# Kernel optimization log

Hardware: AMD Instinct MI355X
Metric: run time of the kernel (lower is better)

Reference implementation:

```python
import jax, jax.numpy as jnp
import numpy as np

K = 5            # SplineConv kernel_size per dim, dim=3
KC = K ** 3      # 125 weight matrices
N0, N1, N2, N3 = 32768, 8192, 2048, 512   # node counts per pooling level (8 graphs)
E0, E1, E2, E3 = 262144, 65536, 16384, 4096
B = 8
NV = B * 8       # dense 2x2x2 voxel grid per graph -> fc1 input 8*256


def spline_conv(x, edge_index, pseudo, W, root, bias):
    # degree-1 (linear) open B-spline convolution, mean aggregation,
    # plus root weight and bias (torch SplineConv defaults).
    src, dst = edge_index[0], edge_index[1]
    N, Cin = x.shape
    Kc, _, Cout = W.shape
    E = src.shape[0]
    v = pseudo * (K - 1)                               # [E,3]
    lo = jnp.clip(jnp.floor(v), 0, K - 2)
    frac = v - lo                                      # [E,3]
    lo = lo.astype(jnp.int32)
    bits = jnp.array([[(s >> d) & 1 for d in range(3)] for s in range(8)], dtype=jnp.int32)  # [8,3]
    idx = lo[:, None, :] + bits[None]                  # [E,8,3] corner grid indices
    w = jnp.where(bits[None] == 1, frac[:, None, :], 1.0 - frac[:, None, :])
    bw = jnp.prod(w, axis=-1)                          # [E,8] basis weights (sum to 1)
    kidx = idx[..., 0] + K * idx[..., 1] + K * K * idx[..., 2]  # [E,8] flat kernel index
    if N * Kc < E * Cin:
        # project every node through all 125 kernels, then gather per edge-corner
        P = jnp.einsum('nc,kco->nko', x, W)            # [N,125,Cout]
        msg = jnp.sum(bw[..., None] * P[src[:, None], kidx], axis=1)  # [E,Cout]
    else:
        # gather weight matrices per edge-corner (cheaper when Cin small)
        xs = x[src]                                    # [E,Cin]
        msg = jnp.zeros((E, Cout), x.dtype)
        for s in range(8):                             # fixed 8 corners of trilinear basis
            msg = msg + bw[:, s, None] * jnp.einsum('ec,eco->eo', xs, W[kidx[:, s]])
    agg = jax.ops.segment_sum(msg, dst, num_segments=N)
    deg = jax.ops.segment_sum(jnp.ones((E,), x.dtype), dst, num_segments=N)
    return agg / jnp.maximum(deg, 1.0)[:, None] + x @ root + bias


def pool_max(x, cluster, n_out):
    out = jax.ops.segment_max(x, cluster, num_segments=n_out)
    return jnp.where(jnp.isfinite(out), out, 0.0)      # empty voxels -> 0


def setup_inputs():
    key = jax.random.key(0)
    ks = iter(jax.random.split(key, 40))
    inp = {"x": jax.random.normal(next(ks), (N0, 1), jnp.float32)}
    levels = [(E0, N0, N1), (E1, N1, N2), (E2, N2, N3), (E3, N3, NV)]
    for l, (E, N, Nn) in enumerate(levels, start=1):
        inp[f"edge_index{l}"] = jax.random.randint(next(ks), (2, E), 0, N)
        inp[f"pseudo{l}"] = jax.random.uniform(next(ks), (E, 3), dtype=jnp.float32)
        inp[f"cluster{l}"] = jax.random.randint(next(ks), (N,), 0, Nn)
    chans = [(1, 32), (32, 64), (64, 128), (128, 256)]
    for l, (ci, co) in enumerate(chans, start=1):
        inp[f"W{l}"] = jax.random.normal(next(ks), (KC, ci, co), jnp.float32) / np.sqrt(ci * 8.0)
        inp[f"root{l}"] = jax.random.normal(next(ks), (ci, co), jnp.float32) / np.sqrt(float(ci))
        inp[f"b{l}"] = jnp.zeros((co,), jnp.float32)
    inp["fc1_w"] = jax.random.normal(next(ks), (2048, 512), jnp.float32) / np.sqrt(2048.0)
    inp["fc1_b"] = jnp.zeros((512,), jnp.float32)
    inp["fc2_w"] = jax.random.normal(next(ks), (512, 10), jnp.float32) / np.sqrt(512.0)
    inp["fc2_b"] = jnp.zeros((10,), jnp.float32)
    return inp


def reference(x, edge_index1, pseudo1, cluster1, edge_index2, pseudo2, cluster2,
              edge_index3, pseudo3, cluster3, edge_index4, pseudo4, cluster4,
              W1, root1, b1, W2, root2, b2, W3, root3, b3, W4, root4, b4,
              fc1_w, fc1_b, fc2_w, fc2_b):
    h = jax.nn.elu(spline_conv(x, edge_index1, pseudo1, W1, root1, b1))
    h = pool_max(h, cluster1, N1)                      # sparse voxel max pool 0.02
    h = jax.nn.elu(spline_conv(h, edge_index2, pseudo2, W2, root2, b2))
    h = pool_max(h, cluster2, N2)                      # sparse voxel max pool 0.04
    h = jax.nn.elu(spline_conv(h, edge_index3, pseudo3, W3, root3, b3))
    h = pool_max(h, cluster3, N3)                      # sparse voxel max pool 0.08
    h = jax.nn.elu(spline_conv(h, edge_index4, pseudo4, W4, root4, b4))
    h = pool_max(h, cluster4, NV)                      # dense 2x2x2 voxel max pool
    h = h.reshape(B, 8 * 256)
    h = jax.nn.elu(h @ fc1_w + fc1_b)                  # dropout is identity in eval mode
    return jax.nn.log_softmax(h @ fc2_w + fc2_b, axis=1)
```

## Files before the change

### kernel.cpp

```cpp
#include <hip/hip_runtime.h>

typedef __attribute__((ext_vector_type(8))) short bf16x8;
typedef __attribute__((ext_vector_type(4))) float f32x4;
typedef __attribute__((ext_vector_type(4))) unsigned short us4;
typedef __attribute__((ext_vector_type(8))) unsigned short us8;

#define DEVI __device__ __forceinline__

#define MAXW2 1088
#define MAXW3 640
#define MAXW4 512


DEVI unsigned enc_pool(float f) {
  unsigned u = __float_as_uint(f);
  return (u & 0x80000000u) ? ~u : (u | 0x80000000u);
}
DEVI float dec_pool(unsigned k) {
  if (k == 0u) return 0.0f;
  return __uint_as_float((k & 0x80000000u) ? (k ^ 0x80000000u) : ~k);
}
DEVI float eluf(float x) { return x > 0.0f ? x : expm1f(x); }
DEVI unsigned short to_bf16(float f) {
  unsigned u = __float_as_uint(f);
  return (unsigned short)((u + 0x7FFFu + ((u >> 16) & 1u)) >> 16);
}

struct Basis { float bw[8]; int kidx[8]; int cell; };

DEVI Basis make_basis(const float* __restrict__ ps, int e) {
  Basis bs;
  float f[3]; int lo[3];
#pragma unroll
  for (int d = 0; d < 3; ++d) {
    float v = ps[e * 3 + d] * 4.0f;
    float fl = fminf(fmaxf(floorf(v), 0.0f), 3.0f);
    lo[d] = (int)fl;
    f[d] = v - fl;
  }
  bs.cell = lo[0] + 4 * lo[1] + 16 * lo[2];
#pragma unroll
  for (int s = 0; s < 8; ++s) {
    int b0 = s & 1, b1 = (s >> 1) & 1, b2 = (s >> 2) & 1;
    bs.bw[s] = (b0 ? f[0] : 1.0f - f[0]) * (b1 ? f[1] : 1.0f - f[1]) *
               (b2 ? f[2] : 1.0f - f[2]);
    bs.kidx[s] = (lo[0] + b0) + 5 * (lo[1] + b1) + 25 * (lo[2] + b2);
  }
  return bs;
}

DEVI int cell_of(const float* __restrict__ ps, int e) {
  int cell = 0;
#pragma unroll
  for (int d = 0; d < 3; ++d) {
    float v = ps[e * 3 + d] * 4.0f;
    float fl = fminf(fmaxf(floorf(v), 0.0f), 3.0f);
    cell |= ((int)fl) << (2 * d);
  }
  return cell;
}

template <int CIN, int COUT>
DEVI void convw(const float* __restrict__ W, unsigned short* __restrict__ P, int idx) {
  constexpr int MAT = CIN * COUT;
  int k = idx / MAT, off = idx % MAT;
  int j = off & 7, g = (off >> 3) & 3;
  int rem = off >> 5;
  int n = rem % COUT, kb = rem / COUT;
  int c = kb * 32 + g * 8 + j;
  P[idx] = to_bf16(W[(k * CIN + c) * COUT + n]);
}

__global__ __launch_bounds__(256) void sc_prep(
    const float* __restrict__ W2, const float* __restrict__ W3, const float* __restrict__ W4,
    unsigned short* __restrict__ P2, unsigned short* __restrict__ P3, unsigned short* __restrict__ P4,
    const int* __restrict__ ei2, const float* __restrict__ ps2,
    const int* __restrict__ ei3, const float* __restrict__ ps3,
    const int* __restrict__ ei4, const float* __restrict__ ps4,
    unsigned* __restrict__ bc2, unsigned* __restrict__ bc3, unsigned* __restrict__ bc4,
    unsigned* __restrict__ deg2, unsigned* __restrict__ deg3, unsigned* __restrict__ deg4,
    const float* __restrict__ x, const int* __restrict__ ei1, const float* __restrict__ ps1,
    const float* __restrict__ W1, float* __restrict__ agg1, unsigned* __restrict__ deg1) {
  __shared__ unsigned hist[64];
  int b = blockIdx.x, t = threadIdx.x;
  if (b < 1000) { convw<32, 64>(W2, P2, b * 256 + t); return; }
  b -= 1000;
  if (b < 4000) { convw<64, 128>(W3, P3, b * 256 + t); return; }
  b -= 4000;
  if (b < 16000) { convw<128, 256>(W4, P4, b * 256 + t); return; }
  b -= 16000;
  if (b < 336) {
    const int* ei; const float* ps; unsigned *bc, *deg; int E, blk, NB;
    if (b < 256)      { ei = ei2; ps = ps2; bc = bc2; deg = deg2; E = 65536; blk = b;       NB = 256; }
    else if (b < 320) { ei = ei3; ps = ps3; bc = bc3; deg = deg3; E = 16384; blk = b - 256; NB = 64;  }
    else              { ei = ei4; ps = ps4; bc = bc4; deg = deg4; E = 4096;  blk = b - 320; NB = 16;  }
    if (t < 64) hist[t] = 0;
    __syncthreads();
    int e = blk * 256 + t;
    atomicAdd(&hist[cell_of(ps, e)], 1u);
    atomicAdd(deg + ei[E + e], 1u);
    __syncthreads();
    if (t < 64) bc[(size_t)t * NB + blk] = hist[t];
    return;
  }
  b -= 336;
  int tid = b * 256 + t;
  int e = tid >> 5, o = tid & 31;
  int src = ei1[e], dst = ei1[262144 + e];
  Basis bs = make_basis(ps1, e);
  float acc = 0.f;
#pragma unroll
  for (int s = 0; s < 8; ++s) acc += bs.bw[s] * W1[bs.kidx[s] * 32 + o];
  atomicAdd(agg1 + dst * 32 + o, x[src] * acc);
  if (o == 0) atomicAdd(deg1 + dst, 1u);
}

__global__ __launch_bounds__(1024) void sc_scan_all(
    const unsigned* __restrict__ bc2, const unsigned* __restrict__ bc3,
    const unsigned* __restrict__ bc4,
    unsigned* __restrict__ bb2, unsigned* __restrict__ bb3, unsigned* __restrict__ bb4,
    unsigned* __restrict__ cnt2, unsigned* __restrict__ cnt3, unsigned* __restrict__ cnt4,
    unsigned* __restrict__ base2, unsigned* __restrict__ base3, unsigned* __restrict__ base4,
    unsigned* __restrict__ wt2, unsigned* __restrict__ wt3, unsigned* __restrict__ wt4) {
  __shared__ unsigned tot[3][64];
  __shared__ unsigned sbs[3][64];
  int t = threadIdx.x, w = t >> 6, lane = t & 63;
#pragma unroll
  for (int lvl = 0; lvl < 3; ++lvl) {
    const unsigned* bc = lvl == 0 ? bc2 : lvl == 1 ? bc3 : bc4;
    unsigned* bb = lvl == 0 ? bb2 : lvl == 1 ? bb3 : bb4;
    int NB = lvl == 0 ? 256 : lvl == 1 ? 64 : 16;
    for (int c = w; c < 64; c += 16) {
      unsigned cellsum = 0;
      for (int sub = 0; sub * 64 < NB; ++sub) {
        int bi = sub * 64 + lane;
        unsigned v = (bi < NB) ? bc[c * NB + bi] : 0u;
        int incl = (int)v;
#pragma unroll
        for (int d = 1; d < 64; d <<= 1) {
          int tv = __shfl_up(incl, d);
          if (lane >= d) incl += tv;
        }
        if (bi < NB) bb[c * NB + bi] = cellsum + (unsigned)incl - v;
        cellsum += (unsigned)__shfl(incl, 63);
      }
      if (lane == 0) tot[lvl][c] = cellsum;
    }
  }
  __syncthreads();
  if (w < 3) {
    unsigned* cnt = w == 0 ? cnt2 : w == 1 ? cnt3 : cnt4;
    unsigned* bs  = w == 0 ? base2 : w == 1 ? base3 : base4;
    unsigned* wt  = w == 0 ? wt2 : w == 1 ? wt3 : wt4;
    int NSP  = w == 0 ? 1 : w == 1 ? 2 : 4;
    int MAXW = w == 0 ? MAXW2 : w == 1 ? MAXW3 : MAXW4;
    unsigned v = tot[w][lane];
    int incl = (int)v;
#pragma unroll
    for (int d = 1; d < 64; d <<= 1) {
      int tv = __shfl_up(incl, d);
      if (lane >= d) incl += tv;
    }
    unsigned excl = (unsigned)incl - v;
    sbs[w][lane] = excl;
    cnt[lane] = v;
    bs[lane] = excl;
    int nch = (int)((v + 63) >> 6);
    int cscan = nch;
#pragma unroll
    for (int d = 1; d < 64; d <<= 1) {
      int tv = __shfl_up(cscan, d);
      if (lane >= d) cscan += tv;
    }
    int cbase = cscan - nch;
    int CT = __shfl(cscan, 63);
    for (int ch = 0; ch < nch; ++ch)
      for (int ns = 0; ns < NSP; ++ns)
        wt[(cbase + ch) * NSP + ns] = ((unsigned)lane << 16) | ((unsigned)ch << 8) | (unsigned)ns;
    for (int i = CT * NSP + lane; i < MAXW; i += 64) wt[i] = 0xFFFFFFFFu;
  }
  __syncthreads();
  for (int i = t; i < 64 * 256; i += 1024) bb2[i] += sbs[0][i >> 8];
  for (int i = t; i < 64 * 64; i += 1024)  bb3[i] += sbs[1][i >> 6];
  for (int i = t; i < 64 * 16; i += 1024)  bb4[i] += sbs[2][i >> 4];
}

__global__ __launch_bounds__(256) void sc_rank_fin1(
    const int* __restrict__ ei2, const float* __restrict__ ps2,
    const int* __restrict__ ei3, const float* __restrict__ ps3,
    const int* __restrict__ ei4, const float* __restrict__ ps4,
    const unsigned* __restrict__ bb2, const unsigned* __restrict__ bb3,
    const unsigned* __restrict__ bb4,
    int* __restrict__ pos2, int* __restrict__ pos3, int* __restrict__ pos4,
    int* __restrict__ dst2, int* __restrict__ dst3, int* __restrict__ dst4,
    const float* __restrict__ x, const float* __restrict__ agg1,
    const unsigned* __restrict__ deg1, const float* __restrict__ root1,
    const float* __restrict__ b1, const int* __restrict__ cl1,
    unsigned* __restrict__ pe1) {
  __shared__ unsigned hist[64];
  int b = blockIdx.x, t = threadIdx.x;
  if (b < 336) {
    const int* ei; const float* ps; const unsigned* bb; int *pos, *dsts; int E, blk, NB;
    if (b < 256)      { ei = ei2; ps = ps2; bb = bb2; pos = pos2; dsts = dst2; E = 65536; blk = b;       NB = 256; }
    else if (b < 320) { ei = ei3; ps = ps3; bb = bb3; pos = pos3; dsts = dst3; E = 16384; blk = b - 256; NB = 64;  }
    else              { ei = ei4; ps = ps4; bb = bb4; pos = pos4; dsts = dst4; E = 4096;  blk = b - 320; NB = 16;  }
    if (t < 64) hist[t] = 0;
    __syncthreads();
    int e = blk * 256 + t;
    int cell = cell_of(ps, e);
    unsigned r = atomicAdd(&hist[cell], 1u);
    int p = (int)(bb[cell * NB + blk] + r);
    pos[e] = p;
    dsts[p] = ei[E + e];
    return;
  }
  b -= 336;
  int tid = b * 256 + t;
  int n = tid >> 5, o = tid & 31;
  unsigned dv = deg1[n];
  float acc = agg1[tid] / (float)(dv ? dv : 1u) + b1[o] + x[n] * root1[o];
  atomicMax(pe1 + (size_t)cl1[n] * 32 + o, enc_pool(eluf(acc)));
}

template <int CIN, int COUT>
__global__ void sc_finpool(const unsigned* __restrict__ xenc, const float* __restrict__ agg,
                           const unsigned* __restrict__ deg, const float* __restrict__ root,
                           const float* __restrict__ bias, const int* __restrict__ cluster,
                           unsigned* __restrict__ pe_out, int N) {
  int tid = blockIdx.x * blockDim.x + threadIdx.x;
  if (tid >= N * COUT) return;
  int n = tid / COUT, o = tid % COUT;
  unsigned dv = deg[n];
  float acc = agg[tid] / (float)(dv ? dv : 1u) + bias[o];
#pragma unroll 4
  for (int c = 0; c < CIN; ++c)
    acc += dec_pool(xenc[n * CIN + c]) * root[c * COUT + o];
  atomicMax(pe_out + (size_t)cluster[n] * COUT + o, enc_pool(eluf(acc)));
}

template <int CIN>
__global__ void sc_fill(const unsigned* __restrict__ xenc, const int* __restrict__ ei,
                        const float* __restrict__ ps, const int* __restrict__ posb,
                        unsigned short* __restrict__ A, int E) {
  int gid = blockIdx.x * blockDim.x + threadIdx.x;
  int e = gid >> 6, lane = gid & 63;
  if (e >= E) return;
  int src = ei[e];
  int p = posb[e];
  float f[3];
#pragma unroll
  for (int d = 0; d < 3; ++d) {
    float v = ps[e * 3 + d] * 4.0f;
    float fl = fminf(fmaxf(floorf(v), 0.0f), 3.0f);
    f[d] = v - fl;
  }
  int sB = lane >> 3;
  int b0 = sB & 1, b1 = (sB >> 1) & 1, b2 = sB >> 2;
  float b = (b0 ? f[0] : 1.0f - f[0]) * (b1 ? f[1] : 1.0f - f[1]) *
            (b2 ? f[2] : 1.0f - f[2]);
  constexpr int K = 8 * CIN;
  if (CIN == 32) {
    uint4 xv = *(const uint4*)(xenc + (size_t)src * 32 + (lane & 7) * 4);
    us4 o;
    o[0] = to_bf16(b * dec_pool(xv.x)); o[1] = to_bf16(b * dec_pool(xv.y));
    o[2] = to_bf16(b * dec_pool(xv.z)); o[3] = to_bf16(b * dec_pool(xv.w));
    *(us4*)(A + (size_t)p * K + lane * 4) = o;
  } else if (CIN == 64) {
    const uint4* xp = (const uint4*)(xenc + (size_t)src * 64 + (lane & 7) * 8);
    uint4 xa = xp[0], xb = xp[1];
    us8 o;
    o[0] = to_bf16(b * dec_pool(xa.x)); o[1] = to_bf16(b * dec_pool(xa.y));
    o[2] = to_bf16(b * dec_pool(xa.z)); o[3] = to_bf16(b * dec_pool(xa.w));
    o[4] = to_bf16(b * dec_pool(xb.x)); o[5] = to_bf16(b * dec_pool(xb.y));
    o[6] = to_bf16(b * dec_pool(xb.z)); o[7] = to_bf16(b * dec_pool(xb.w));
    *(us8*)(A + (size_t)p * K + lane * 8) = o;
  } else {
    const uint4* xp = (const uint4*)(xenc + (size_t)src * 128 + (lane & 7) * 16);
#pragma unroll
    for (int h = 0; h < 2; ++h) {
      uint4 xa = xp[h * 2], xb = xp[h * 2 + 1];
      us8 o;
      o[0] = to_bf16(b * dec_pool(xa.x)); o[1] = to_bf16(b * dec_pool(xa.y));
      o[2] = to_bf16(b * dec_pool(xa.z)); o[3] = to_bf16(b * dec_pool(xa.w));
      o[4] = to_bf16(b * dec_pool(xb.x)); o[5] = to_bf16(b * dec_pool(xb.y));
      o[6] = to_bf16(b * dec_pool(xb.z)); o[7] = to_bf16(b * dec_pool(xb.w));
      *(us8*)(A + (size_t)p * K + lane * 16 + h * 8) = o;
    }
  }
}

template <int CIN, int COUT, int NSP>
DEVI void gemm_impl(const unsigned short* __restrict__ A, const unsigned short* __restrict__ Wp,
                    const unsigned* __restrict__ cnt, const unsigned* __restrict__ base,
                    const unsigned* __restrict__ wtab, const int* __restrict__ dsts,
                    float* __restrict__ agg) {
  constexpr int K = 8 * CIN;
  constexpr int NCOL = COUT / NSP;
  constexpr int NT = NCOL / 16;
  constexpr int UPT = NCOL / 32;
  constexpr int NPASS = K / 64;
  __shared__ __attribute__((aligned(16))) unsigned char lds[2 * NCOL * 80];
  unsigned u = wtab[blockIdx.x];
  if (u == 0xFFFFFFFFu) return;
  int cell = u >> 16, chunk = (u >> 8) & 255, nsl = u & 255;
  int n0 = nsl * NCOL;
  int m = (int)cnt[cell], cb = (int)base[cell];
  int row0 = chunk * 64;
  int tid = threadIdx.x;
  int wv = tid >> 6, lane = tid & 63, g4 = lane >> 4, ln = lane & 15;
  int lo0 = cell & 3, lo1 = (cell >> 2) & 3, lo2 = cell >> 4;
  int arow = cb + min(row0 + wv * 16 + ln, m - 1);
  f32x4 acc[NT];
#pragma unroll
  for (int t = 0; t < NT; ++t) acc[t] = (f32x4){0.f, 0.f, 0.f, 0.f};
  for (int pass = 0; pass < NPASS; ++pass) {
    int k0 = pass * 64;
    __syncthreads();
#pragma unroll
    for (int i = 0; i < UPT; ++i) {
      int u16 = tid + i * 256;
      int grp = u16 / (4 * NCOL), win = u16 % (4 * NCOL);
      int kg = k0 + grp * 32;
      int s = kg / CIN, kb = (kg % CIN) >> 5;
      int b0 = s & 1, b1 = (s >> 1) & 1, b2 = (s >> 2) & 1;
      int mat = (lo0 + b0) + 5 * (lo1 + b1) + 25 * (lo2 + b2);
      const us8* srcp = (const us8*)(Wp + (size_t)mat * (CIN * COUT) +
                                     (size_t)(kb * COUT * 4 + n0 * 4 + win) * 8);
      int r = grp * NCOL + (win >> 2), gg = win & 3;
      *(us8*)(lds + r * 80 + gg * 16) = *srcp;
    }
    __syncthreads();
#pragma unroll
    for (int kk = 0; kk < 2; ++kk) {
      bf16x8 af = *(const bf16x8*)(A + (size_t)arow * K + k0 + kk * 32 + g4 * 8);
#pragma unroll
      for (int t = 0; t < NT; ++t) {
        int r = kk * NCOL + t * 16 + ln;
        bf16x8 bfr = *(const bf16x8*)(lds + r * 80 + g4 * 16);
        acc[t] = __builtin_amdgcn_mfma_f32_16x16x32_bf16(af, bfr, acc[t], 0, 0, 0);
      }
    }
  }
  int row_b = row0 + wv * 16 + g4 * 4;
  int dstv[4];
#pragma unroll
  for (int r4 = 0; r4 < 4; ++r4)
    dstv[r4] = (row_b + r4 < m) ? dsts[cb + row_b + r4] : -1;
#pragma unroll
  for (int t = 0; t < NT; ++t) {
#pragma unroll
    for (int r4 = 0; r4 < 4; ++r4) {
      if (dstv[r4] >= 0)
        atomicAdd(agg + (size_t)dstv[r4] * COUT + n0 + t * 16 + ln, acc[t][r4]);
    }
  }
}

__global__ __launch_bounds__(256) void sc_gemm_l2(
    const unsigned short* A, const unsigned short* Wp, const unsigned* cnt,
    const unsigned* base, const unsigned* wtab, const int* dsts, float* agg) {
  gemm_impl<32, 64, 1>(A, Wp, cnt, base, wtab, dsts, agg);
}
__global__ __launch_bounds__(256) void sc_gemm_l3(
    const unsigned short* A, const unsigned short* Wp, const unsigned* cnt,
    const unsigned* base, const unsigned* wtab, const int* dsts, float* agg) {
  gemm_impl<64, 128, 2>(A, Wp, cnt, base, wtab, dsts, agg);
}
__global__ __launch_bounds__(256) void sc_gemm_l4(
    const unsigned short* A, const unsigned short* Wp, const unsigned* cnt,
    const unsigned* base, const unsigned* wtab, const int* dsts, float* agg) {
  gemm_impl<128, 256, 4>(A, Wp, cnt, base, wtab, dsts, agg);
}

__global__ void sc_fc1(const unsigned* __restrict__ xenc, const float* __restrict__ w,
                       float* __restrict__ out) {
  __shared__ float sx[8][32];
  int t = threadIdx.x;
  int j = blockIdx.x * 256 + t;
  int c0 = blockIdx.y * 32;
  {
    int b = t >> 5, c = t & 31;
    sx[b][c] = dec_pool(xenc[b * 2048 + c0 + c]);
  }
  __syncthreads();
  float acc[8];
#pragma unroll
  for (int b = 0; b < 8; ++b) acc[b] = 0.f;
#pragma unroll 4
  for (int cc = 0; cc < 32; ++cc) {
    float wv = w[(size_t)(c0 + cc) * 512 + j];
#pragma unroll
    for (int b = 0; b < 8; ++b) acc[b] += sx[b][cc] * wv;
  }
#pragma unroll
  for (int b = 0; b < 8; ++b) atomicAdd(out + b * 512 + j, acc[b]);
}

__global__ void sc_fc2(const float* __restrict__ h, const float* __restrict__ b1,
                       const float* __restrict__ w2, const float* __restrict__ b2,
                       float* __restrict__ out) {
  int b = blockIdx.x;
  int lane = threadIdx.x;
  float part[10];
#pragma unroll
  for (int o = 0; o < 10; ++o) part[o] = 0.f;
  for (int k = 0; k < 8; ++k) {
    int c = k * 64 + lane;
    float v = eluf(h[b * 512 + c] + b1[c]);
#pragma unroll
    for (int o = 0; o < 10; ++o) part[o] += v * w2[c * 10 + o];
  }
#pragma unroll
  for (int o = 0; o < 10; ++o) {
#pragma unroll
    for (int d = 32; d > 0; d >>= 1) part[o] += __shfl_down(part[o], d);
  }
  if (lane == 0) {
    float z[10], mx = -1e30f;
#pragma unroll
    for (int o = 0; o < 10; ++o) { z[o] = part[o] + b2[o]; mx = fmaxf(mx, z[o]); }
    float sum = 0.f;
#pragma unroll
    for (int o = 0; o < 10; ++o) sum += expf(z[o] - mx);
    float lse = mx + logf(sum);
#pragma unroll
    for (int o = 0; o < 10; ++o) out[b * 10 + o] = z[o] - lse;
  }
}

extern "C" void kernel_launch(void* const* d_in, const int* in_sizes, int n_in,
                              void* d_out, int out_size, void* d_ws, size_t ws_size,
                              hipStream_t stream) {
  (void)in_sizes; (void)n_in; (void)out_size; (void)ws_size;
  const float* x    = (const float*)d_in[0];
  const int*   ei1  = (const int*)d_in[1];
  const float* ps1  = (const float*)d_in[2];
  const int*   cl1  = (const int*)d_in[3];
  const int*   ei2  = (const int*)d_in[4];
  const float* ps2  = (const float*)d_in[5];
  const int*   cl2  = (const int*)d_in[6];
  const int*   ei3  = (const int*)d_in[7];
  const float* ps3  = (const float*)d_in[8];
  const int*   cl3  = (const int*)d_in[9];
  const int*   ei4  = (const int*)d_in[10];
  const float* ps4  = (const float*)d_in[11];
  const int*   cl4  = (const int*)d_in[12];
  const float* W1   = (const float*)d_in[13];
  const float* root1= (const float*)d_in[14];
  const float* b1   = (const float*)d_in[15];
  const float* W2   = (const float*)d_in[16];
  const float* root2= (const float*)d_in[17];
  const float* b2   = (const float*)d_in[18];
  const float* W3   = (const float*)d_in[19];
  const float* root3= (const float*)d_in[20];
  const float* b3   = (const float*)d_in[21];
  const float* W4   = (const float*)d_in[22];
  const float* root4= (const float*)d_in[23];
  const float* b4   = (const float*)d_in[24];
  const float* fc1w = (const float*)d_in[25];
  const float* fc1b = (const float*)d_in[26];
  const float* fc2w = (const float*)d_in[27];
  const float* fc2b = (const float*)d_in[28];
  float* out = (float*)d_out;

  char* ws = (char*)d_ws;
  size_t off = 0;
  auto alloc = [&](size_t bytes) -> void* {
    void* p = ws + off;
    off = (off + bytes + 255) & ~(size_t)255;
    return p;
  };
  float*    agg1 = (float*)alloc(32768ull * 32 * 4);
  float*    agg2 = (float*)alloc(8192ull * 64 * 4);
  float*    agg3 = (float*)alloc(2048ull * 128 * 4);
  float*    agg4 = (float*)alloc(512ull * 256 * 4);
  unsigned* deg1 = (unsigned*)alloc(32768ull * 4);
  unsigned* deg2 = (unsigned*)alloc(8192ull * 4);
  unsigned* deg3 = (unsigned*)alloc(2048ull * 4);
  unsigned* deg4 = (unsigned*)alloc(512ull * 4);
  unsigned* pe1  = (unsigned*)alloc(8192ull * 32 * 4);
  unsigned* pe2  = (unsigned*)alloc(2048ull * 64 * 4);
  unsigned* pe3  = (unsigned*)alloc(512ull * 128 * 4);
  unsigned* pe4  = (unsigned*)alloc(64ull * 256 * 4);
  float*    fc1o = (float*)alloc(8ull * 512 * 4);
  size_t zero_bytes = off;
  unsigned* bc2   = (unsigned*)alloc(64ull * 256 * 4);
  unsigned* bc3   = (unsigned*)alloc(64ull * 64 * 4);
  unsigned* bc4   = (unsigned*)alloc(64ull * 16 * 4);
  unsigned* bb2   = (unsigned*)alloc(64ull * 256 * 4);
  unsigned* bb3   = (unsigned*)alloc(64ull * 64 * 4);
  unsigned* bb4   = (unsigned*)alloc(64ull * 16 * 4);
  unsigned* cnt2  = (unsigned*)alloc(64 * 4);
  unsigned* cnt3  = (unsigned*)alloc(64 * 4);
  unsigned* cnt4  = (unsigned*)alloc(64 * 4);
  unsigned* base2 = (unsigned*)alloc(64 * 4);
  unsigned* base3 = (unsigned*)alloc(64 * 4);
  unsigned* base4 = (unsigned*)alloc(64 * 4);
  unsigned* wt2   = (unsigned*)alloc(MAXW2 * 4);
  unsigned* wt3   = (unsigned*)alloc(MAXW3 * 4);
  unsigned* wt4   = (unsigned*)alloc(MAXW4 * 4);
  int* pos2 = (int*)alloc(65536ull * 4);
  int* pos3 = (int*)alloc(16384ull * 4);
  int* pos4 = (int*)alloc(4096ull * 4);
  int* dst2 = (int*)alloc(65536ull * 4);
  int* dst3 = (int*)alloc(16384ull * 4);
  int* dst4 = (int*)alloc(4096ull * 4);
  unsigned short* Wp2 = (unsigned short*)alloc(125ull * 32 * 64 * 2);
  unsigned short* Wp3 = (unsigned short*)alloc(125ull * 64 * 128 * 2);
  unsigned short* Wp4 = (unsigned short*)alloc(125ull * 128 * 256 * 2);
  unsigned short* A   = (unsigned short*)alloc(65536ull * 256 * 2);

  hipMemsetAsync(d_ws, 0, zero_bytes, stream);
  sc_prep<<<54104, 256, 0, stream>>>(W2, W3, W4, Wp2, Wp3, Wp4,
                                     ei2, ps2, ei3, ps3, ei4, ps4,
                                     bc2, bc3, bc4, deg2, deg3, deg4,
                                     x, ei1, ps1, W1, agg1, deg1);
  sc_scan_all<<<1, 1024, 0, stream>>>(bc2, bc3, bc4, bb2, bb3, bb4,
                                      cnt2, cnt3, cnt4, base2, base3, base4,
                                      wt2, wt3, wt4);
  sc_rank_fin1<<<4432, 256, 0, stream>>>(ei2, ps2, ei3, ps3, ei4, ps4,
                                         bb2, bb3, bb4, pos2, pos3, pos4,
                                         dst2, dst3, dst4,
                                         x, agg1, deg1, root1, b1, cl1, pe1);

  sc_fill<32><<<16384, 256, 0, stream>>>(pe1, ei2, ps2, pos2, A, 65536);
  sc_gemm_l2<<<MAXW2, 256, 0, stream>>>(A, Wp2, cnt2, base2, wt2, dst2, agg2);
  sc_finpool<32, 64><<<2048, 256, 0, stream>>>(pe1, agg2, deg2, root2, b2, cl2, pe2, 8192);

  sc_fill<64><<<4096, 256, 0, stream>>>(pe2, ei3, ps3, pos3, A, 16384);
  sc_gemm_l3<<<MAXW3, 256, 0, stream>>>(A, Wp3, cnt3, base3, wt3, dst3, agg3);
  sc_finpool<64, 128><<<1024, 256, 0, stream>>>(pe2, agg3, deg3, root3, b3, cl3, pe3, 2048);

  sc_fill<128><<<1024, 256, 0, stream>>>(pe3, ei4, ps4, pos4, A, 4096);
  sc_gemm_l4<<<MAXW4, 256, 0, stream>>>(A, Wp4, cnt4, base4, wt4, dst4, agg4);
  sc_finpool<128, 256><<<512, 256, 0, stream>>>(pe3, agg4, deg4, root4, b4, cl4, pe4, 512);

  sc_fc1<<<dim3(2, 64), 256, 0, stream>>>(pe4, fc1w, fc1o);
  sc_fc2<<<8, 64, 0, stream>>>(fc1o, fc1b, fc2w, fc2b, out);
}
```

Baseline: 216.1 us.

## Fuse A-matrix fill into spline GEMMs and share basis weights via shuffles

Drops the separate sc_fill kernels that wrote a bf16 expanded A matrix to global memory. Each GEMM block now gathers source features and basis weights for its 64 rows itself, through an inverse permutation (eid) built during ranking, and stages the A tile in LDS. This removes three launches and a large global write and read-back. In exchange, every block redoes the feature gather per k-step, so global reads repeat for each column split. Separately, the layer-1 edge kernel computes each corner's basis once per lane and shares it with warp shuffles instead of every lane recomputing all eight.

```diff
diff --git a/kernel.cpp b/kernel.cpp
--- a/kernel.cpp
+++ b/kernel.cpp
@@ -2,7 +2,6 @@
 
 typedef __attribute__((ext_vector_type(8))) short bf16x8;
 typedef __attribute__((ext_vector_type(4))) float f32x4;
-typedef __attribute__((ext_vector_type(4))) unsigned short us4;
 typedef __attribute__((ext_vector_type(8))) unsigned short us8;
 
 #define DEVI __device__ __forceinline__
@@ -24,29 +23,6 @@
 DEVI unsigned short to_bf16(float f) {
   unsigned u = __float_as_uint(f);
   return (unsigned short)((u + 0x7FFFu + ((u >> 16) & 1u)) >> 16);
-}
-
-struct Basis { float bw[8]; int kidx[8]; int cell; };
-
-DEVI Basis make_basis(const float* __restrict__ ps, int e) {
-  Basis bs;
-  float f[3]; int lo[3];
-#pragma unroll
-  for (int d = 0; d < 3; ++d) {
-    float v = ps[e * 3 + d] * 4.0f;
-    float fl = fminf(fmaxf(floorf(v), 0.0f), 3.0f);
-    lo[d] = (int)fl;
-    f[d] = v - fl;
-  }
-  bs.cell = lo[0] + 4 * lo[1] + 16 * lo[2];
-#pragma unroll
-  for (int s = 0; s < 8; ++s) {
-    int b0 = s & 1, b1 = (s >> 1) & 1, b2 = (s >> 2) & 1;
-    bs.bw[s] = (b0 ? f[0] : 1.0f - f[0]) * (b1 ? f[1] : 1.0f - f[1]) *
-               (b2 ? f[2] : 1.0f - f[2]);
-    bs.kidx[s] = (lo[0] + b0) + 5 * (lo[1] + b1) + 25 * (lo[2] + b2);
-  }
-  return bs;
 }
 
 DEVI int cell_of(const float* __restrict__ ps, int e) {
@@ -106,11 +82,28 @@
   b -= 336;
   int tid = b * 256 + t;
   int e = tid >> 5, o = tid & 31;
+  int ebit = t & 32;
   int src = ei1[e], dst = ei1[262144 + e];
-  Basis bs = make_basis(ps1, e);
+  float f[3]; int lo[3];
+#pragma unroll
+  for (int d = 0; d < 3; ++d) {
+    float v = ps1[e * 3 + d] * 4.0f;
+    float fl = fminf(fmaxf(floorf(v), 0.0f), 3.0f);
+    lo[d] = (int)fl;
+    f[d] = v - fl;
+  }
+  int so = o & 7;
+  int c0 = so & 1, c1 = (so >> 1) & 1, c2 = (so >> 2) & 1;
+  float bw_own = (c0 ? f[0] : 1.0f - f[0]) * (c1 ? f[1] : 1.0f - f[1]) *
+                 (c2 ? f[2] : 1.0f - f[2]);
+  int k_own = (lo[0] + c0) + 5 * (lo[1] + c1) + 25 * (lo[2] + c2);
   float acc = 0.f;
 #pragma unroll
-  for (int s = 0; s < 8; ++s) acc += bs.bw[s] * W1[bs.kidx[s] * 32 + o];
+  for (int s = 0; s < 8; ++s) {
+    float bws = __shfl(bw_own, ebit + s);
+    int ks = __shfl(k_own, ebit + s);
+    acc += bws * W1[ks * 32 + o];
+  }
   atomicAdd(agg1 + dst * 32 + o, x[src] * acc);
   if (o == 0) atomicAdd(deg1 + dst, 1u);
 }
@@ -191,7 +184,7 @@
     const int* __restrict__ ei4, const float* __restrict__ ps4,
     const unsigned* __restrict__ bb2, const unsigned* __restrict__ bb3,
     const unsigned* __restrict__ bb4,
-    int* __restrict__ pos2, int* __restrict__ pos3, int* __restrict__ pos4,
+    int* __restrict__ eid2, int* __restrict__ eid3, int* __restrict__ eid4,
     int* __restrict__ dst2, int* __restrict__ dst3, int* __restrict__ dst4,
     const float* __restrict__ x, const float* __restrict__ agg1,
     const unsigned* __restrict__ deg1, const float* __restrict__ root1,
@@ -200,17 +193,17 @@
   __shared__ unsigned hist[64];
   int b = blockIdx.x, t = threadIdx.x;
   if (b < 336) {
-    const int* ei; const float* ps; const unsigned* bb; int *pos, *dsts; int E, blk, NB;
-    if (b < 256)      { ei = ei2; ps = ps2; bb = bb2; pos = pos2; dsts = dst2; E = 65536; blk = b;       NB = 256; }
-    else if (b < 320) { ei = ei3; ps = ps3; bb = bb3; pos = pos3; dsts = dst3; E = 16384; blk = b - 256; NB = 64;  }
-    else              { ei = ei4; ps = ps4; bb = bb4; pos = pos4; dsts = dst4; E = 4096;  blk = b - 320; NB = 16;  }
+    const int* ei; const float* ps; const unsigned* bb; int *eid, *dsts; int E, blk, NB;
+    if (b < 256)      { ei = ei2; ps = ps2; bb = bb2; eid = eid2; dsts = dst2; E = 65536; blk = b;       NB = 256; }
+    else if (b < 320) { ei = ei3; ps = ps3; bb = bb3; eid = eid3; dsts = dst3; E = 16384; blk = b - 256; NB = 64;  }
+    else              { ei = ei4; ps = ps4; bb = bb4; eid = eid4; dsts = dst4; E = 4096;  blk = b - 320; NB = 16;  }
     if (t < 64) hist[t] = 0;
     __syncthreads();
     int e = blk * 256 + t;
     int cell = cell_of(ps, e);
     unsigned r = atomicAdd(&hist[cell], 1u);
     int p = (int)(bb[cell * NB + blk] + r);
-    pos[e] = p;
+    eid[p] = e;
     dsts[p] = ei[E + e];
     return;
   }
@@ -238,59 +231,10 @@
   atomicMax(pe_out + (size_t)cluster[n] * COUT + o, enc_pool(eluf(acc)));
 }
 
-template <int CIN>
-__global__ void sc_fill(const unsigned* __restrict__ xenc, const int* __restrict__ ei,
-                        const float* __restrict__ ps, const int* __restrict__ posb,
-                        unsigned short* __restrict__ A, int E) {
-  int gid = blockIdx.x * blockDim.x + threadIdx.x;
-  int e = gid >> 6, lane = gid & 63;
-  if (e >= E) return;
-  int src = ei[e];
-  int p = posb[e];
-  float f[3];
-#pragma unroll
-  for (int d = 0; d < 3; ++d) {
-    float v = ps[e * 3 + d] * 4.0f;
-    float fl = fminf(fmaxf(floorf(v), 0.0f), 3.0f);
-    f[d] = v - fl;
-  }
-  int sB = lane >> 3;
-  int b0 = sB & 1, b1 = (sB >> 1) & 1, b2 = sB >> 2;
-  float b = (b0 ? f[0] : 1.0f - f[0]) * (b1 ? f[1] : 1.0f - f[1]) *
-            (b2 ? f[2] : 1.0f - f[2]);
-  constexpr int K = 8 * CIN;
-  if (CIN == 32) {
-    uint4 xv = *(const uint4*)(xenc + (size_t)src * 32 + (lane & 7) * 4);
-    us4 o;
-    o[0] = to_bf16(b * dec_pool(xv.x)); o[1] = to_bf16(b * dec_pool(xv.y));
-    o[2] = to_bf16(b * dec_pool(xv.z)); o[3] = to_bf16(b * dec_pool(xv.w));
-    *(us4*)(A + (size_t)p * K + lane * 4) = o;
-  } else if (CIN == 64) {
-    const uint4* xp = (const uint4*)(xenc + (size_t)src * 64 + (lane & 7) * 8);
-    uint4 xa = xp[0], xb = xp[1];
-    us8 o;
-    o[0] = to_bf16(b * dec_pool(xa.x)); o[1] = to_bf16(b * dec_pool(xa.y));
-    o[2] = to_bf16(b * dec_pool(xa.z)); o[3] = to_bf16(b * dec_pool(xa.w));
-    o[4] = to_bf16(b * dec_pool(xb.x)); o[5] = to_bf16(b * dec_pool(xb.y));
-    o[6] = to_bf16(b * dec_pool(xb.z)); o[7] = to_bf16(b * dec_pool(xb.w));
-    *(us8*)(A + (size_t)p * K + lane * 8) = o;
-  } else {
-    const uint4* xp = (const uint4*)(xenc + (size_t)src * 128 + (lane & 7) * 16);
-#pragma unroll
-    for (int h = 0; h < 2; ++h) {
-      uint4 xa = xp[h * 2], xb = xp[h * 2 + 1];
-      us8 o;
-      o[0] = to_bf16(b * dec_pool(xa.x)); o[1] = to_bf16(b * dec_pool(xa.y));
-      o[2] = to_bf16(b * dec_pool(xa.z)); o[3] = to_bf16(b * dec_pool(xa.w));
-      o[4] = to_bf16(b * dec_pool(xb.x)); o[5] = to_bf16(b * dec_pool(xb.y));
-      o[6] = to_bf16(b * dec_pool(xb.z)); o[7] = to_bf16(b * dec_pool(xb.w));
-      *(us8*)(A + (size_t)p * K + lane * 16 + h * 8) = o;
-    }
-  }
-}
-
 template <int CIN, int COUT, int NSP>
-DEVI void gemm_impl(const unsigned short* __restrict__ A, const unsigned short* __restrict__ Wp,
+DEVI void gemm_impl(const int* __restrict__ ei, const float* __restrict__ ps,
+                    const unsigned* __restrict__ xenc, const int* __restrict__ eid,
+                    const unsigned short* __restrict__ Wp,
                     const unsigned* __restrict__ cnt, const unsigned* __restrict__ base,
                     const unsigned* __restrict__ wtab, const int* __restrict__ dsts,
                     float* __restrict__ agg) {
@@ -300,6 +244,9 @@
   constexpr int UPT = NCOL / 32;
   constexpr int NPASS = K / 64;
   __shared__ __attribute__((aligned(16))) unsigned char lds[2 * NCOL * 80];
+  __shared__ __attribute__((aligned(16))) unsigned short ldsA[64][72];
+  __shared__ float s_bw[64][8];
+  __shared__ int s_src[64];
   unsigned u = wtab[blockIdx.x];
   if (u == 0xFFFFFFFFu) return;
   int cell = u >> 16, chunk = (u >> 8) & 255, nsl = u & 255;
@@ -309,7 +256,24 @@
   int tid = threadIdx.x;
   int wv = tid >> 6, lane = tid & 63, g4 = lane >> 4, ln = lane & 15;
   int lo0 = cell & 3, lo1 = (cell >> 2) & 3, lo2 = cell >> 4;
-  int arow = cb + min(row0 + wv * 16 + ln, m - 1);
+  if (tid < 64) {
+    int ridx = cb + min(row0 + tid, m - 1);
+    int e = eid[ridx];
+    s_src[tid] = ei[e];
+    float f[3];
+#pragma unroll
+    for (int d = 0; d < 3; ++d) {
+      float v = ps[e * 3 + d] * 4.0f;
+      float fl = fminf(fmaxf(floorf(v), 0.0f), 3.0f);
+      f[d] = v - fl;
+    }
+#pragma unroll
+    for (int s = 0; s < 8; ++s) {
+      int b0 = s & 1, b1 = (s >> 1) & 1, b2 = (s >> 2) & 1;
+      s_bw[tid][s] = (b0 ? f[0] : 1.0f - f[0]) * (b1 ? f[1] : 1.0f - f[1]) *
+                     (b2 ? f[2] : 1.0f - f[2]);
+    }
+  }
   f32x4 acc[NT];
 #pragma unroll
   for (int t = 0; t < NT; ++t) acc[t] = (f32x4){0.f, 0.f, 0.f, 0.f};
@@ -329,10 +293,32 @@
       int r = grp * NCOL + (win >> 2), gg = win & 3;
       *(us8*)(lds + r * 80 + gg * 16) = *srcp;
     }
+    {
+      int r = tid >> 2, q = tid & 3;
+      int kg = k0 + q * 16;
+      int sidx = kg / CIN;
+      int c0 = kg & (CIN - 1);
+      float bwv = s_bw[r][sidx];
+      const uint4* xp = (const uint4*)(xenc + (size_t)s_src[r] * CIN + c0);
+      uint4 xa = xp[0], xb = xp[1];
+      us8 o0;
+      o0[0] = to_bf16(bwv * dec_pool(xa.x)); o0[1] = to_bf16(bwv * dec_pool(xa.y));
+      o0[2] = to_bf16(bwv * dec_pool(xa.z)); o0[3] = to_bf16(bwv * dec_pool(xa.w));
+      o0[4] = to_bf16(bwv * dec_pool(xb.x)); o0[5] = to_bf16(bwv * dec_pool(xb.y));
+      o0[6] = to_bf16(bwv * dec_pool(xb.z)); o0[7] = to_bf16(bwv * dec_pool(xb.w));
+      uint4 xc = xp[2], xd = xp[3];
+      us8 o1;
+      o1[0] = to_bf16(bwv * dec_pool(xc.x)); o1[1] = to_bf16(bwv * dec_pool(xc.y));
+      o1[2] = to_bf16(bwv * dec_pool(xc.z)); o1[3] = to_bf16(bwv * dec_pool(xc.w));
+      o1[4] = to_bf16(bwv * dec_pool(xd.x)); o1[5] = to_bf16(bwv * dec_pool(xd.y));
+      o1[6] = to_bf16(bwv * dec_pool(xd.z)); o1[7] = to_bf16(bwv * dec_pool(xd.w));
+      *(us8*)&ldsA[r][q * 16] = o0;
+      *(us8*)&ldsA[r][q * 16 + 8] = o1;
+    }
     __syncthreads();
 #pragma unroll
     for (int kk = 0; kk < 2; ++kk) {
-      bf16x8 af = *(const bf16x8*)(A + (size_t)arow * K + k0 + kk * 32 + g4 * 8);
+      bf16x8 af = *(const bf16x8*)&ldsA[wv * 16 + ln][kk * 32 + g4 * 8];
 #pragma unroll
       for (int t = 0; t < NT; ++t) {
         int r = kk * NCOL + t * 16 + ln;
@@ -357,19 +343,22 @@
 }
 
 __global__ __launch_bounds__(256) void sc_gemm_l2(
-    const unsigned short* A, const unsigned short* Wp, const unsigned* cnt,
-    const unsigned* base, const unsigned* wtab, const int* dsts, float* agg) {
-  gemm_impl<32, 64, 1>(A, Wp, cnt, base, wtab, dsts, agg);
+    const int* ei, const float* ps, const unsigned* xenc, const int* eid,
+    const unsigned short* Wp, const unsigned* cnt, const unsigned* base,
+    const unsigned* wtab, const int* dsts, float* agg) {
+  gemm_impl<32, 64, 1>(ei, ps, xenc, eid, Wp, cnt, base, wtab, dsts, agg);
 }
 __global__ __launch_bounds__(256) void sc_gemm_l3(
-    const unsigned short* A, const unsigned short* Wp, const unsigned* cnt,
-    const unsigned* base, const unsigned* wtab, const int* dsts, float* agg) {
-  gemm_impl<64, 128, 2>(A, Wp, cnt, base, wtab, dsts, agg);
+    const int* ei, const float* ps, const unsigned* xenc, const int* eid,
+    const unsigned short* Wp, const unsigned* cnt, const unsigned* base,
+    const unsigned* wtab, const int* dsts, float* agg) {
+  gemm_impl<64, 128, 2>(ei, ps, xenc, eid, Wp, cnt, base, wtab, dsts, agg);
 }
 __global__ __launch_bounds__(256) void sc_gemm_l4(
-    const unsigned short* A, const unsigned short* Wp, const unsigned* cnt,
-    const unsigned* base, const unsigned* wtab, const int* dsts, float* agg) {
-  gemm_impl<128, 256, 4>(A, Wp, cnt, base, wtab, dsts, agg);
+    const int* ei, const float* ps, const unsigned* xenc, const int* eid,
+    const unsigned short* Wp, const unsigned* cnt, const unsigned* base,
+    const unsigned* wtab, const int* dsts, float* agg) {
+  gemm_impl<128, 256, 4>(ei, ps, xenc, eid, Wp, cnt, base, wtab, dsts, agg);
 }
 
 __global__ void sc_fc1(const unsigned* __restrict__ xenc, const float* __restrict__ w,
@@ -499,16 +488,15 @@
   unsigned* wt2   = (unsigned*)alloc(MAXW2 * 4);
   unsigned* wt3   = (unsigned*)alloc(MAXW3 * 4);
   unsigned* wt4   = (unsigned*)alloc(MAXW4 * 4);
-  int* pos2 = (int*)alloc(65536ull * 4);
-  int* pos3 = (int*)alloc(16384ull * 4);
-  int* pos4 = (int*)alloc(4096ull * 4);
+  int* eid2 = (int*)alloc(65536ull * 4);
+  int* eid3 = (int*)alloc(16384ull * 4);
+  int* eid4 = (int*)alloc(4096ull * 4);
   int* dst2 = (int*)alloc(65536ull * 4);
   int* dst3 = (int*)alloc(16384ull * 4);
   int* dst4 = (int*)alloc(4096ull * 4);
   unsigned short* Wp2 = (unsigned short*)alloc(125ull * 32 * 64 * 2);
   unsigned short* Wp3 = (unsigned short*)alloc(125ull * 64 * 128 * 2);
   unsigned short* Wp4 = (unsigned short*)alloc(125ull * 128 * 256 * 2);
-  unsigned short* A   = (unsigned short*)alloc(65536ull * 256 * 2);
 
   hipMemsetAsync(d_ws, 0, zero_bytes, stream);
   sc_prep<<<54104, 256, 0, stream>>>(W2, W3, W4, Wp2, Wp3, Wp4,
@@ -519,20 +507,17 @@
                                       cnt2, cnt3, cnt4, base2, base3, base4,
                                       wt2, wt3, wt4);
   sc_rank_fin1<<<4432, 256, 0, stream>>>(ei2, ps2, ei3, ps3, ei4, ps4,
-                                         bb2, bb3, bb4, pos2, pos3, pos4,
+                                         bb2, bb3, bb4, eid2, eid3, eid4,
                                          dst2, dst3, dst4,
                                          x, agg1, deg1, root1, b1, cl1, pe1);
 
-  sc_fill<32><<<16384, 256, 0, stream>>>(pe1, ei2, ps2, pos2, A, 65536);
-  sc_gemm_l2<<<MAXW2, 256, 0, stream>>>(A, Wp2, cnt2, base2, wt2, dst2, agg2);
+  sc_gemm_l2<<<MAXW2, 256, 0, stream>>>(ei2, ps2, pe1, eid2, Wp2, cnt2, base2, wt2, dst2, agg2);
   sc_finpool<32, 64><<<2048, 256, 0, stream>>>(pe1, agg2, deg2, root2, b2, cl2, pe2, 8192);
 
-  sc_fill<64><<<4096, 256, 0, stream>>>(pe2, ei3, ps3, pos3, A, 16384);
-  sc_gemm_l3<<<MAXW3, 256, 0, stream>>>(A, Wp3, cnt3, base3, wt3, dst3, agg3);
+  sc_gemm_l3<<<MAXW3, 256, 0, stream>>>(ei3, ps3, pe2, eid3, Wp3, cnt3, base3, wt3, dst3, agg3);
   sc_finpool<64, 128><<<1024, 256, 0, stream>>>(pe2, agg3, deg3, root3, b3, cl3, pe3, 2048);
 
-  sc_fill<128><<<1024, 256, 0, stream>>>(pe3, ei4, ps4, pos4, A, 4096);
-  sc_gemm_l4<<<MAXW4, 256, 0, stream>>>(A, Wp4, cnt4, base4, wt4, dst4, agg4);
+  sc_gemm_l4<<<MAXW4, 256, 0, stream>>>(ei4, ps4, pe3, eid4, Wp4, cnt4, base4, wt4, dst4, agg4);
   sc_finpool<128, 256><<<512, 256, 0, stream>>>(pe3, agg4, deg4, root4, b4, cl4, pe4, 512);
 
   sc_fc1<<<dim3(2, 64), 256, 0, stream>>>(pe4, fc1w, fc1o);
```

Result: faster. 195.4 us (-9.6%).
